# Optimization experiments

Hardware: AMD Instinct MI355X
Metric: run time of the kernel (lower is better)

## Reference

```python
import jax, jax.numpy as jnp
import numpy as np

D = 768          # hidden_size
M = 8            # num_patchmerges
B = 16
S = 2048         # non-CLF tokens


def setup_inputs() -> dict:
    key = jax.random.key(0)
    ks = jax.random.split(key, 12)
    std = 0.02
    tokens = jax.random.normal(ks[0], (B, 1 + S, D), dtype=jnp.float32)
    lengths = jnp.maximum(jax.random.randint(ks[1], (B,), 0, S), 1).astype(jnp.int64)
    # PatchMerger: learned queries + layernorm params
    q = jax.random.normal(ks[2], (M, D), dtype=jnp.float32) * std
    ln_scale = jnp.ones((D,), dtype=jnp.float32)
    ln_bias = jnp.zeros((D,), dtype=jnp.float32)
    # mlp1: Linear(3D, D) -> GELU -> Linear(D, D)
    w1a = jax.random.normal(ks[3], (3 * D, D), dtype=jnp.float32) * std
    b1a = jnp.zeros((D,), dtype=jnp.float32)
    w2a = jax.random.normal(ks[4], (D, D), dtype=jnp.float32) * std
    b2a = jnp.zeros((D,), dtype=jnp.float32)
    # mlp2: Linear((1+M)D, D) -> GELU -> Linear(D, D)
    w1b = jax.random.normal(ks[5], ((1 + M) * D, D), dtype=jnp.float32) * std
    b1b = jnp.zeros((D,), dtype=jnp.float32)
    w2b = jax.random.normal(ks[6], (D, D), dtype=jnp.float32) * std
    b2b = jnp.zeros((D,), dtype=jnp.float32)
    return dict(tokens=tokens, lengths=lengths, q=q, ln_scale=ln_scale,
                ln_bias=ln_bias, w1a=w1a, b1a=b1a, w2a=w2a, b2a=b2a,
                w1b=w1b, b1b=b1b, w2b=w2b, b2b=b2b)


def _hpmlp(x, w1, b1, w2, b2):
    h = jax.nn.gelu(x @ w1 + b1, approximate=False)  # dropout=0 -> identity
    return h @ w2 + b2


def _layernorm(x, scale, bias, eps=1e-5):
    mu = jnp.mean(x, axis=-1, keepdims=True)
    var = jnp.var(x, axis=-1, keepdims=True)
    return (x - mu) * jax.lax.rsqrt(var + eps) * scale + bias


def reference(tokens, lengths, q, ln_scale, ln_bias,
              w1a, b1a, w2a, b2a, w1b, b1b, w2b, b2b):
    clf = tokens[:, 0]            # [B, D]
    x = tokens[:, 1:]             # [B, S, D]
    mask = jnp.arange(S)[None, :] < lengths[:, None]   # [B, S]
    mf = mask[..., None].astype(x.dtype)

    # fixed path: masked mean / max / min over valid tokens
    denom = lengths.astype(x.dtype)[:, None]
    mean_p = jnp.sum(x * mf, axis=1) / denom
    max_p = jnp.max(jnp.where(mask[..., None], x, -jnp.inf), axis=1)
    min_p = jnp.min(jnp.where(mask[..., None], x, jnp.inf), axis=1)
    pooled_trad = jnp.concatenate([mean_p, max_p, min_p], axis=-1)  # [B, 3D]
    out_fixed = _hpmlp(pooled_trad, w1a, b1a, w2a, b2a)

    # learned path: PatchMerger (masked attention from M learned queries)
    xn = _layernorm(x, ln_scale, ln_bias)
    scores = jnp.einsum('md,bsd->bms', q, xn) / jnp.sqrt(jnp.asarray(D, x.dtype))
    scores = jnp.where(mask[:, None, :], scores, -jnp.inf)
    attn = jax.nn.softmax(scores, axis=-1)                # [B, M, S]
    merged = jnp.einsum('bms,bsd->bmd', attn, x)          # [B, M, D]
    pooled_learn = jnp.concatenate([merged.reshape(B, M * D), clf], axis=-1)
    out_learn = _hpmlp(pooled_learn, w1b, b1b, w2b, b2b)

    return jnp.concatenate([out_fixed, out_learn], axis=-1)  # [B, 2D]
```

## Files before the change

### kernel.cpp

```cpp
#include <hip/hip_runtime.h>
#include <math.h>

#define SD 768
#define SB 16
#define SM 8
#define SS 2048
#define TOK_ROW 2049
#define NEG_INF (-__builtin_inff())

#define OFF_PTRADS  0
#define OFF_PLEARN  36864
#define OFF_LTOT    147456
#define OFF_P1A     147584
#define OFF_P1B     368768
#define OFF_HA      1032320
#define OFF_HB      1044608
#define OFF_CNT     1056896

#define NITEM 512

__device__ __forceinline__ int clen(int v) { return v < 1 ? 1 : (v > SS ? SS : v); }

__device__ __forceinline__ unsigned fenc(float f) {
  unsigned u = __float_as_uint(f);
  return (u & 0x80000000u) ? ~u : (u ^ 0x80000000u);
}
__device__ __forceinline__ float fdec(unsigned u) {
  unsigned i = (u & 0x80000000u) ? (u ^ 0x80000000u) : ~u;
  return __uint_as_float(i);
}

__global__ void k_init(float* __restrict__ ws, float* __restrict__ out,
                       const float* __restrict__ b2a, const float* __restrict__ b2b) {
  int i = blockIdx.x * 256 + threadIdx.x;
  int stride = gridDim.x * 256;
  for (int t = i; t < 147584; t += stride) {
    unsigned v = (t >= 24576 && t < 36864) ? 0xFFFFFFFFu : 0u;
    ((unsigned*)ws)[t] = v;
  }
  for (int t = i; t < 24576; t += stride) {
    int b = t / 1536, r = t - b * 1536;
    out[t] = (r < 768) ? b2a[r] : b2b[r - 768];
  }
  if (i == 0) ((int*)ws)[OFF_CNT] = 0;
}

__global__ __launch_bounds__(512, 1) void k_fused(
    const float* __restrict__ tokens, const int* __restrict__ lengths,
    const float* __restrict__ q, const float* __restrict__ lns,
    const float* __restrict__ lnb, float* __restrict__ ptradS,
    float* __restrict__ plearn, float* __restrict__ ltot,
    int* __restrict__ cnt) {
  __shared__ float q_lds[8][SD];
  __shared__ float O_lds[SM][SD];
  __shared__ float pool_lds[8][3][SD];
  __shared__ float l_lds[8][8];
  __shared__ float qmeta[16];
  __shared__ int item_s;
  int tid = threadIdx.x, w = tid >> 6, lane = tid & 63;
  int mm2 = lane & 3;

  {
    float s1 = 0.f, sb = 0.f;
    #pragma unroll
    for (int g = 0; g < 3; ++g) {
      float4 l4  = *(const float4*)(lns + g * 256 + lane * 4);
      float4 lb4 = *(const float4*)(lnb + g * 256 + lane * 4);
      float4 qv  = *(const float4*)(q + w * SD + g * 256 + lane * 4);
      float4 qs = make_float4(qv.x * l4.x, qv.y * l4.y, qv.z * l4.z, qv.w * l4.w);
      *(float4*)&q_lds[w][g * 256 + lane * 4] = qs;
      s1 += qs.x + qs.y + qs.z + qs.w;
      sb += qv.x * lb4.x + qv.y * lb4.y + qv.z * lb4.z + qv.w * lb4.w;
    }
    #pragma unroll
    for (int o = 32; o; o >>= 1) { s1 += __shfl_xor(s1, o, 64); sb += __shfl_xor(sb, o, 64); }
    if (lane == 0) { qmeta[w] = s1; qmeta[8 + w] = sb; }
  }
  __syncthreads();
  float qs1A = qmeta[mm2],     qs1B = qmeta[4 + mm2];
  float qbA  = qmeta[8 + mm2], qbB  = qmeta[12 + mm2];
  const float KS = 0.03608439182435161f;

  for (;;) {
    __syncthreads();
    if (tid == 0) item_s = atomicAdd(cnt, 1);
    __syncthreads();
    int item = item_s;
    if (item >= NITEM) break;
    int b = item >> 5, c = item & 31;
    int len = clen(lengths[b]);
    int c0 = c * 64;
    if (c0 >= len) continue;

    int srow = c0 + w * 8;
    int smax = len - srow; if (smax > 8) smax = 8; if (smax < 0) smax = 0;
    const float* xrow = tokens + ((size_t)b * TOK_ROW + 1 + srow) * SD;

    float psum[12], pmx[12], pmn[12];
    #pragma unroll
    for (int j = 0; j < 12; ++j) { psum[j] = 0.f; pmx[j] = NEG_INF; pmn[j] = -NEG_INF; }
    float O[8][12];
    #pragma unroll
    for (int m = 0; m < 8; ++m)
      #pragma unroll
      for (int j = 0; j < 12; ++j) O[m][j] = 0.f;
    float lA = 0.f, lB = 0.f;

    float4 nx0 = {}, nx1 = {}, nx2 = {};
    if (smax > 0) {
      nx0 = *(const float4*)(xrow + lane * 4);
      nx1 = *(const float4*)(xrow + 256 + lane * 4);
      nx2 = *(const float4*)(xrow + 512 + lane * 4);
    }
    for (int i = 0; i < smax; ++i) {
      float4 x0 = nx0, x1 = nx1, x2 = nx2;
      if (i + 1 < smax) {
        const float* xq = xrow + (size_t)(i + 1) * SD;
        nx0 = *(const float4*)(xq + lane * 4);
        nx1 = *(const float4*)(xq + 256 + lane * 4);
        nx2 = *(const float4*)(xq + 512 + lane * 4);
      }
      float xv[12] = {x0.x, x0.y, x0.z, x0.w, x1.x, x1.y, x1.z, x1.w,
                      x2.x, x2.y, x2.z, x2.w};
      float s1 = 0.f, s2 = 0.f;
      #pragma unroll
      for (int j = 0; j < 12; ++j) {
        float v = xv[j];
        psum[j] += v;
        pmx[j] = fmaxf(pmx[j], v);
        pmn[j] = fminf(pmn[j], v);
        s1 += v;
        s2 += v * v;
      }
      float d[8];
      #pragma unroll
      for (int m = 0; m < 8; ++m) {
        float4 q0 = *(const float4*)&q_lds[m][lane * 4];
        float4 q1 = *(const float4*)&q_lds[m][256 + lane * 4];
        float4 q2 = *(const float4*)&q_lds[m][512 + lane * 4];
        d[m] = q0.x * xv[0] + q0.y * xv[1] + q0.z * xv[2] + q0.w * xv[3]
             + q1.x * xv[4] + q1.y * xv[5] + q1.z * xv[6] + q1.w * xv[7]
             + q2.x * xv[8] + q2.y * xv[9] + q2.z * xv[10] + q2.w * xv[11];
      }
      #pragma unroll
      for (int o = 1; o <= 2; o <<= 1)
        #pragma unroll
        for (int m = 0; m < 8; ++m) d[m] += __shfl_xor(d[m], o, 64);
      float uA = d[0], uB = d[4];
      #pragma unroll
      for (int m = 1; m < 4; ++m) {
        uA = (mm2 == m) ? d[m] : uA;
        uB = (mm2 == m) ? d[4 + m] : uB;
      }
      #pragma unroll
      for (int o = 4; o <= 32; o <<= 1) {
        uA += __shfl_xor(uA, o, 64);
        uB += __shfl_xor(uB, o, 64);
        s1 += __shfl_xor(s1, o, 64);
        s2 += __shfl_xor(s2, o, 64);
      }
      #pragma unroll
      for (int o = 1; o <= 2; o <<= 1) { s1 += __shfl_xor(s1, o, 64); s2 += __shfl_xor(s2, o, 64); }
      float mu = s1 * (1.f / 768.f);
      float var = s2 * (1.f / 768.f) - mu * mu;
      float rstd = rsqrtf(var + 1e-5f);
      float peA = __expf((rstd * uA - rstd * mu * qs1A + qbA) * KS);
      float peB = __expf((rstd * uB - rstd * mu * qs1B + qbB) * KS);
      lA += peA; lB += peB;
      float pm[8];
      #pragma unroll
      for (int m = 0; m < 4; ++m) {
        pm[m]     = __shfl(peA, m, 4);
        pm[4 + m] = __shfl(peB, m, 4);
      }
      #pragma unroll
      for (int m = 0; m < 8; ++m)
        #pragma unroll
        for (int j = 0; j < 12; ++j) O[m][j] += pm[m] * xv[j];
    }

    if (lane < 4) { l_lds[w][lane] = lA; l_lds[w][4 + lane] = lB; }
    #pragma unroll
    for (int g = 0; g < 3; ++g) {
      int dd = g * 256 + lane * 4;
      *(float4*)&pool_lds[w][0][dd] = make_float4(psum[g*4], psum[g*4+1], psum[g*4+2], psum[g*4+3]);
      *(float4*)&pool_lds[w][1][dd] = make_float4(pmx[g*4], pmx[g*4+1], pmx[g*4+2], pmx[g*4+3]);
      *(float4*)&pool_lds[w][2][dd] = make_float4(pmn[g*4], pmn[g*4+1], pmn[g*4+2], pmn[g*4+3]);
    }
    __syncthreads();

    if (tid < 8) {
      float lt = 0.f;
      #pragma unroll
      for (int ww = 0; ww < 8; ++ww) lt += l_lds[ww][tid];
      atomicAdd(&ltot[b * 8 + tid], lt);
    }

    #pragma unroll
    for (int r = 0; r < 8; ++r) {
      if (w == r) {
        #pragma unroll
        for (int m = 0; m < 8; ++m)
          #pragma unroll
          for (int g = 0; g < 3; ++g) {
            int dd = g * 256 + lane * 4;
            float4 mine = make_float4(O[m][g*4], O[m][g*4+1], O[m][g*4+2], O[m][g*4+3]);
            if (r == 0) {
              *(float4*)&O_lds[m][dd] = mine;
            } else {
              float4 cur = *(float4*)&O_lds[m][dd];
              cur.x += mine.x; cur.y += mine.y; cur.z += mine.z; cur.w += mine.w;
              *(float4*)&O_lds[m][dd] = cur;
            }
          }
      }
      __syncthreads();
    }

    {
      const float* of = &O_lds[0][0];
      for (int j = tid; j < 6144; j += 512)
        atomicAdd(&plearn[(size_t)b * 6912 + j], of[j]);
    }
    for (int j = tid; j < 768; j += 512) {
      float s = 0.f, mx = NEG_INF, mn = -NEG_INF;
      #pragma unroll
      for (int ww = 0; ww < 8; ++ww) {
        s += pool_lds[ww][0][j];
        mx = fmaxf(mx, pool_lds[ww][1][j]);
        mn = fminf(mn, pool_lds[ww][2][j]);
      }
      atomicAdd(&ptradS[b * 768 + j], s);
      atomicMax((unsigned*)&ptradS[12288 + b * 768 + j], fenc(mx));
      atomicMin((unsigned*)&ptradS[24576 + b * 768 + j], fenc(mn));
    }
    if (c == 0)
      for (int dd = tid; dd < 768; dd += 512)
        plearn[(size_t)b * 6912 + 6144 + dd] = tokens[(size_t)b * TOK_ROW * SD + dd];
  }
}

__global__ __launch_bounds__(256) void gemm_partial(
    const float* __restrict__ XA, const float* __restrict__ WA, int ktA, float* __restrict__ PA,
    const float* __restrict__ XB, const float* __restrict__ WB, float* __restrict__ PB,
    const int* __restrict__ lengths, const float* __restrict__ ltot,
    int modeA, int modeB, int epi) {
  int nt = blockIdx.x, ky = blockIdx.y;
  const float *X, *W; float* P; int kt, ktN, mode;
  if (ky < ktA) { X = XA; W = WA; P = PA; kt = ky; ktN = ktA; mode = modeA; }
  else { X = XB; W = WB; P = PB; kt = ky - ktA; ktN = gridDim.y - ktA; mode = modeB; }
  int K = ktN * 128;
  int k0 = kt * 128;
  __shared__ __align__(16) float xt[128 * 20];
  __shared__ float red[4][64][17];
  int tid = threadIdx.x;
  int kk = tid & 127, half = tid >> 7;
  #pragma unroll
  for (int u = 0; u < 8; ++u) {
    int b2 = half * 8 + u;
    float f;
    if (mode == 0) {
      int s = kt / 6;
      f = X[s * 12288 + b2 * 768 + (k0 - s * 768) + kk];
      if (s == 0) f = f / (float)clen(lengths[b2]);
      else        f = fdec(__float_as_uint(f));
    } else if (mode == 1) {
      f = X[b2 * 6912 + k0 + kk];
      if (kt < 48) f = f / ltot[b2 * 8 + (k0 / 768)];
    } else {
      f = X[b2 * K + k0 + kk];
    }
    xt[kk * 20 + b2] = f;
  }
  __syncthreads();
  int w = tid >> 6, lane = tid & 63;
  int n = nt * 64 + lane;
  float acc[16];
  #pragma unroll
  for (int b2 = 0; b2 < 16; ++b2) acc[b2] = 0.f;
  const float* Wp = W + (size_t)k0 * SD + n;
  #pragma unroll 8
  for (int kj = 0; kj < 32; ++kj) {
    int k = w + kj * 4;
    float wv = Wp[(size_t)k * SD];
    const float4* xr = reinterpret_cast<const float4*>(xt + k * 20);
    float4 a0 = xr[0], a1 = xr[1], a2 = xr[2], a3 = xr[3];
    acc[0] += wv * a0.x; acc[1] += wv * a0.y; acc[2] += wv * a0.z; acc[3] += wv * a0.w;
    acc[4] += wv * a1.x; acc[5] += wv * a1.y; acc[6] += wv * a1.z; acc[7] += wv * a1.w;
    acc[8] += wv * a2.x; acc[9] += wv * a2.y; acc[10] += wv * a2.z; acc[11] += wv * a2.w;
    acc[12] += wv * a3.x; acc[13] += wv * a3.y; acc[14] += wv * a3.z; acc[15] += wv * a3.w;
  }
  #pragma unroll
  for (int b2 = 0; b2 < 16; ++b2) red[w][lane][b2] = acc[b2];
  __syncthreads();
  for (int i = tid; i < 1024; i += 256) {
    int nn = i & 63, b2 = i >> 6;
    float r = red[0][nn][b2] + red[1][nn][b2] + red[2][nn][b2] + red[3][nn][b2];
    if (epi == 0) P[(size_t)(kt * 16 + b2) * SD + nt * 64 + nn] = r;
    else          atomicAdd(&P[b2 * 1536 + nt * 64 + nn], r);
  }
}

__global__ void gelu_reduce(const float* __restrict__ PA, const float* __restrict__ b1a,
                            float* __restrict__ HA, const float* __restrict__ PB,
                            const float* __restrict__ b1b, float* __restrict__ HB) {
  int y = blockIdx.y;
  int j = blockIdx.x * 256 + threadIdx.x;
  float r;
  if (y == 0) {
    r = b1a[j % SD];
    #pragma unroll
    for (int kt = 0; kt < 18; ++kt) r += PA[kt * 12288 + j];
    HA[j] = r * 0.5f * (1.f + erff(r * 0.70710678118654752f));
  } else {
    r = b1b[j % SD];
    #pragma unroll
    for (int kt = 0; kt < 54; ++kt) r += PB[kt * 12288 + j];
    HB[j] = r * 0.5f * (1.f + erff(r * 0.70710678118654752f));
  }
}

extern "C" void kernel_launch(void* const* d_in, const int* in_sizes, int n_in,
                              void* d_out, int out_size, void* d_ws, size_t ws_size,
                              hipStream_t stream) {
  const float* tokens = (const float*)d_in[0];
  const int* lengths  = (const int*)d_in[1];
  const float* q      = (const float*)d_in[2];
  const float* lns    = (const float*)d_in[3];
  const float* lnb    = (const float*)d_in[4];
  const float* w1a    = (const float*)d_in[5];
  const float* b1a    = (const float*)d_in[6];
  const float* w2a    = (const float*)d_in[7];
  const float* b2a    = (const float*)d_in[8];
  const float* w1b    = (const float*)d_in[9];
  const float* b1b    = (const float*)d_in[10];
  const float* w2b    = (const float*)d_in[11];
  const float* b2b    = (const float*)d_in[12];
  float* ws  = (float*)d_ws;
  float* out = (float*)d_out;

  float* ptradS = ws + OFF_PTRADS;
  float* plearn = ws + OFF_PLEARN;
  float* ltot   = ws + OFF_LTOT;
  float* p1a    = ws + OFF_P1A;
  float* p1b    = ws + OFF_P1B;
  float* ha     = ws + OFF_HA;
  float* hb     = ws + OFF_HB;
  int*   cnt    = (int*)(ws + OFF_CNT);

  k_init<<<dim3(128), 256, 0, stream>>>(ws, out, b2a, b2b);
  k_fused<<<dim3(256), 512, 0, stream>>>(tokens, lengths, q, lns, lnb,
                                         ptradS, plearn, ltot, cnt);
  gemm_partial<<<dim3(12, 72), 256, 0, stream>>>(ptradS, w1a, 18, p1a,
                                                 plearn, w1b, p1b,
                                                 lengths, ltot, 0, 1, 0);
  gelu_reduce<<<dim3(48, 2), 256, 0, stream>>>(p1a, b1a, ha, p1b, b1b, hb);
  gemm_partial<<<dim3(12, 12), 256, 0, stream>>>(ha, w2a, 6, out,
                                                 hb, w2b, out + 768,
                                                 lengths, ltot, 2, 2, 1);
}
```

Measured before the change: 239.1 us.

## Pin fused blocks to one batch and fold GELU reduce into second GEMM

Each fused block now serves a fixed batch (blockIdx mod 16) and pulls chunks from a per-batch atomic counter. It keeps its accumulators across chunks and does the cross-wave reduction and global atomics once at the end instead of once per chunk, which cuts atomic traffic and per-chunk LDS reductions. The separate gelu_reduce kernel is removed: the second GEMM's tile loader sums the split-K partials, adds the bias and applies GELU inline. The trade-off is that batches with short lengths leave their 16 blocks idle while long batches still have only 16 blocks each, so load balance gets worse. The second GEMM also recomputes the partial reductions redundantly across its tiles.

```diff
diff --git a/kernel.cpp b/kernel.cpp
--- a/kernel.cpp
+++ b/kernel.cpp
@@ -13,11 +13,7 @@
 #define OFF_LTOT    147456
 #define OFF_P1A     147584
 #define OFF_P1B     368768
-#define OFF_HA      1032320
-#define OFF_HB      1044608
-#define OFF_CNT     1056896
-
-#define NITEM 512
+#define OFF_CNT     1032320
 
 __device__ __forceinline__ int clen(int v) { return v < 1 ? 1 : (v > SS ? SS : v); }
 
@@ -42,7 +38,7 @@
     int b = t / 1536, r = t - b * 1536;
     out[t] = (r < 768) ? b2a[r] : b2b[r - 768];
   }
-  if (i == 0) ((int*)ws)[OFF_CNT] = 0;
+  if (i < 16) ((int*)(ws + OFF_CNT))[i] = 0;
 }
 
 __global__ __launch_bounds__(512, 1) void k_fused(
@@ -52,13 +48,15 @@
     float* __restrict__ plearn, float* __restrict__ ltot,
     int* __restrict__ cnt) {
   __shared__ float q_lds[8][SD];
-  __shared__ float O_lds[SM][SD];
-  __shared__ float pool_lds[8][3][SD];
+  __shared__ float scr[8][SD];
   __shared__ float l_lds[8][8];
   __shared__ float qmeta[16];
-  __shared__ int item_s;
+  __shared__ int chunk_s;
   int tid = threadIdx.x, w = tid >> 6, lane = tid & 63;
   int mm2 = lane & 3;
+  int b = blockIdx.x & 15;
+  int len = clen(lengths[b]);
+  int nch = (len + 63) >> 6;
 
   {
     float s1 = 0.f, sb = 0.f;
@@ -81,30 +79,30 @@
   float qbA  = qmeta[8 + mm2], qbB  = qmeta[12 + mm2];
   const float KS = 0.03608439182435161f;
 
+  float psum[12], pmx[12], pmn[12];
+  #pragma unroll
+  for (int j = 0; j < 12; ++j) { psum[j] = 0.f; pmx[j] = NEG_INF; pmn[j] = -NEG_INF; }
+  float O[8][12];
+  #pragma unroll
+  for (int m = 0; m < 8; ++m)
+    #pragma unroll
+    for (int j = 0; j < 12; ++j) O[m][j] = 0.f;
+  float lA = 0.f, lB = 0.f;
+  int ndone = 0;
+  bool have_c0 = false;
+
   for (;;) {
     __syncthreads();
-    if (tid == 0) item_s = atomicAdd(cnt, 1);
-    __syncthreads();
-    int item = item_s;
-    if (item >= NITEM) break;
-    int b = item >> 5, c = item & 31;
-    int len = clen(lengths[b]);
-    int c0 = c * 64;
-    if (c0 >= len) continue;
-
-    int srow = c0 + w * 8;
+    if (tid == 0) chunk_s = atomicAdd(&cnt[b], 1);
+    __syncthreads();
+    int c = chunk_s;
+    if (c >= nch) break;
+    ++ndone;
+    if (c == 0) have_c0 = true;
+
+    int srow = c * 64 + w * 8;
     int smax = len - srow; if (smax > 8) smax = 8; if (smax < 0) smax = 0;
     const float* xrow = tokens + ((size_t)b * TOK_ROW + 1 + srow) * SD;
-
-    float psum[12], pmx[12], pmn[12];
-    #pragma unroll
-    for (int j = 0; j < 12; ++j) { psum[j] = 0.f; pmx[j] = NEG_INF; pmn[j] = -NEG_INF; }
-    float O[8][12];
-    #pragma unroll
-    for (int m = 0; m < 8; ++m)
-      #pragma unroll
-      for (int j = 0; j < 12; ++j) O[m][j] = 0.f;
-    float lA = 0.f, lB = 0.f;
 
     float4 nx0 = {}, nx1 = {}, nx2 = {};
     if (smax > 0) {
@@ -178,77 +176,77 @@
         #pragma unroll
         for (int j = 0; j < 12; ++j) O[m][j] += pm[m] * xv[j];
     }
-
-    if (lane < 4) { l_lds[w][lane] = lA; l_lds[w][4 + lane] = lB; }
+  }
+
+  if (ndone == 0) return;
+
+  #pragma unroll
+  for (int m = 0; m < 8; ++m) {
+    __syncthreads();
+    #pragma unroll
+    for (int g = 0; g < 3; ++g)
+      *(float4*)&scr[w][g * 256 + lane * 4] =
+          make_float4(O[m][g*4], O[m][g*4+1], O[m][g*4+2], O[m][g*4+3]);
+    __syncthreads();
+    for (int ch = tid; ch < 768; ch += 512) {
+      float s = scr[0][ch] + scr[1][ch] + scr[2][ch] + scr[3][ch]
+              + scr[4][ch] + scr[5][ch] + scr[6][ch] + scr[7][ch];
+      atomicAdd(&plearn[(size_t)b * 6912 + m * 768 + ch], s);
+    }
+  }
+  #pragma unroll
+  for (int st = 0; st < 3; ++st) {
+    __syncthreads();
     #pragma unroll
     for (int g = 0; g < 3; ++g) {
       int dd = g * 256 + lane * 4;
-      *(float4*)&pool_lds[w][0][dd] = make_float4(psum[g*4], psum[g*4+1], psum[g*4+2], psum[g*4+3]);
-      *(float4*)&pool_lds[w][1][dd] = make_float4(pmx[g*4], pmx[g*4+1], pmx[g*4+2], pmx[g*4+3]);
-      *(float4*)&pool_lds[w][2][dd] = make_float4(pmn[g*4], pmn[g*4+1], pmn[g*4+2], pmn[g*4+3]);
-    }
-    __syncthreads();
-
-    if (tid < 8) {
-      float lt = 0.f;
-      #pragma unroll
-      for (int ww = 0; ww < 8; ++ww) lt += l_lds[ww][tid];
-      atomicAdd(&ltot[b * 8 + tid], lt);
-    }
-
-    #pragma unroll
-    for (int r = 0; r < 8; ++r) {
-      if (w == r) {
-        #pragma unroll
-        for (int m = 0; m < 8; ++m)
-          #pragma unroll
-          for (int g = 0; g < 3; ++g) {
-            int dd = g * 256 + lane * 4;
-            float4 mine = make_float4(O[m][g*4], O[m][g*4+1], O[m][g*4+2], O[m][g*4+3]);
-            if (r == 0) {
-              *(float4*)&O_lds[m][dd] = mine;
-            } else {
-              float4 cur = *(float4*)&O_lds[m][dd];
-              cur.x += mine.x; cur.y += mine.y; cur.z += mine.z; cur.w += mine.w;
-              *(float4*)&O_lds[m][dd] = cur;
-            }
-          }
-      }
-      __syncthreads();
-    }
-
-    {
-      const float* of = &O_lds[0][0];
-      for (int j = tid; j < 6144; j += 512)
-        atomicAdd(&plearn[(size_t)b * 6912 + j], of[j]);
-    }
-    for (int j = tid; j < 768; j += 512) {
-      float s = 0.f, mx = NEG_INF, mn = -NEG_INF;
-      #pragma unroll
-      for (int ww = 0; ww < 8; ++ww) {
-        s += pool_lds[ww][0][j];
-        mx = fmaxf(mx, pool_lds[ww][1][j]);
-        mn = fminf(mn, pool_lds[ww][2][j]);
-      }
-      atomicAdd(&ptradS[b * 768 + j], s);
-      atomicMax((unsigned*)&ptradS[12288 + b * 768 + j], fenc(mx));
-      atomicMin((unsigned*)&ptradS[24576 + b * 768 + j], fenc(mn));
-    }
-    if (c == 0)
-      for (int dd = tid; dd < 768; dd += 512)
-        plearn[(size_t)b * 6912 + 6144 + dd] = tokens[(size_t)b * TOK_ROW * SD + dd];
-  }
+      float4 v;
+      if (st == 0)      v = make_float4(psum[g*4], psum[g*4+1], psum[g*4+2], psum[g*4+3]);
+      else if (st == 1) v = make_float4(pmx[g*4], pmx[g*4+1], pmx[g*4+2], pmx[g*4+3]);
+      else              v = make_float4(pmn[g*4], pmn[g*4+1], pmn[g*4+2], pmn[g*4+3]);
+      *(float4*)&scr[w][dd] = v;
+    }
+    __syncthreads();
+    for (int ch = tid; ch < 768; ch += 512) {
+      if (st == 0) {
+        float s = scr[0][ch] + scr[1][ch] + scr[2][ch] + scr[3][ch]
+                + scr[4][ch] + scr[5][ch] + scr[6][ch] + scr[7][ch];
+        atomicAdd(&ptradS[b * 768 + ch], s);
+      } else if (st == 1) {
+        float s = fmaxf(fmaxf(fmaxf(scr[0][ch], scr[1][ch]), fmaxf(scr[2][ch], scr[3][ch])),
+                        fmaxf(fmaxf(scr[4][ch], scr[5][ch]), fmaxf(scr[6][ch], scr[7][ch])));
+        atomicMax((unsigned*)&ptradS[12288 + b * 768 + ch], fenc(s));
+      } else {
+        float s = fminf(fminf(fminf(scr[0][ch], scr[1][ch]), fminf(scr[2][ch], scr[3][ch])),
+                        fminf(fminf(scr[4][ch], scr[5][ch]), fminf(scr[6][ch], scr[7][ch])));
+        atomicMin((unsigned*)&ptradS[24576 + b * 768 + ch], fenc(s));
+      }
+    }
+  }
+  __syncthreads();
+  if (lane < 4) { l_lds[w][lane] = lA; l_lds[w][4 + lane] = lB; }
+  __syncthreads();
+  if (tid < 8) {
+    float lt = 0.f;
+    #pragma unroll
+    for (int ww = 0; ww < 8; ++ww) lt += l_lds[ww][tid];
+    atomicAdd(&ltot[b * 8 + tid], lt);
+  }
+  if (have_c0)
+    for (int dd = tid; dd < 768; dd += 512)
+      plearn[(size_t)b * 6912 + 6144 + dd] = tokens[(size_t)b * TOK_ROW * SD + dd];
 }
 
 __global__ __launch_bounds__(256) void gemm_partial(
     const float* __restrict__ XA, const float* __restrict__ WA, int ktA, float* __restrict__ PA,
     const float* __restrict__ XB, const float* __restrict__ WB, float* __restrict__ PB,
     const int* __restrict__ lengths, const float* __restrict__ ltot,
+    const float* __restrict__ bA, const float* __restrict__ bB,
     int modeA, int modeB, int epi) {
   int nt = blockIdx.x, ky = blockIdx.y;
-  const float *X, *W; float* P; int kt, ktN, mode;
-  if (ky < ktA) { X = XA; W = WA; P = PA; kt = ky; ktN = ktA; mode = modeA; }
-  else { X = XB; W = WB; P = PB; kt = ky - ktA; ktN = gridDim.y - ktA; mode = modeB; }
+  const float *X, *W, *bias; float* P; int kt, ktN, mode;
+  if (ky < ktA) { X = XA; W = WA; P = PA; kt = ky; ktN = ktA; mode = modeA; bias = bA; }
+  else { X = XB; W = WB; P = PB; kt = ky - ktA; ktN = gridDim.y - ktA; mode = modeB; bias = bB; }
   int K = ktN * 128;
   int k0 = kt * 128;
   __shared__ __align__(16) float xt[128 * 20];
@@ -268,7 +266,17 @@
       f = X[b2 * 6912 + k0 + kk];
       if (kt < 48) f = f / ltot[b2 * 8 + (k0 / 768)];
     } else {
-      f = X[b2 * K + k0 + kk];
+      int k = k0 + kk;
+      const float* Pp = X + b2 * 768 + k;
+      f = bias[k];
+      if (mode == 3) {
+        #pragma unroll
+        for (int t = 0; t < 18; ++t) f += Pp[t * 12288];
+      } else {
+        #pragma unroll 6
+        for (int t = 0; t < 54; ++t) f += Pp[t * 12288];
+      }
+      f = f * 0.5f * (1.f + erff(f * 0.70710678118654752f));
     }
     xt[kk * 20 + b2] = f;
   }
@@ -298,25 +306,6 @@
     float r = red[0][nn][b2] + red[1][nn][b2] + red[2][nn][b2] + red[3][nn][b2];
     if (epi == 0) P[(size_t)(kt * 16 + b2) * SD + nt * 64 + nn] = r;
     else          atomicAdd(&P[b2 * 1536 + nt * 64 + nn], r);
-  }
-}
-
-__global__ void gelu_reduce(const float* __restrict__ PA, const float* __restrict__ b1a,
-                            float* __restrict__ HA, const float* __restrict__ PB,
-                            const float* __restrict__ b1b, float* __restrict__ HB) {
-  int y = blockIdx.y;
-  int j = blockIdx.x * 256 + threadIdx.x;
-  float r;
-  if (y == 0) {
-    r = b1a[j % SD];
-    #pragma unroll
-    for (int kt = 0; kt < 18; ++kt) r += PA[kt * 12288 + j];
-    HA[j] = r * 0.5f * (1.f + erff(r * 0.70710678118654752f));
-  } else {
-    r = b1b[j % SD];
-    #pragma unroll
-    for (int kt = 0; kt < 54; ++kt) r += PB[kt * 12288 + j];
-    HB[j] = r * 0.5f * (1.f + erff(r * 0.70710678118654752f));
   }
 }
 
@@ -344,8 +333,6 @@
   float* ltot   = ws + OFF_LTOT;
   float* p1a    = ws + OFF_P1A;
   float* p1b    = ws + OFF_P1B;
-  float* ha     = ws + OFF_HA;
-  float* hb     = ws + OFF_HB;
   int*   cnt    = (int*)(ws + OFF_CNT);
 
   k_init<<<dim3(128), 256, 0, stream>>>(ws, out, b2a, b2b);
@@ -353,9 +340,8 @@
                                          ptradS, plearn, ltot, cnt);
   gemm_partial<<<dim3(12, 72), 256, 0, stream>>>(ptradS, w1a, 18, p1a,
                                                  plearn, w1b, p1b,
-                                                 lengths, ltot, 0, 1, 0);
-  gelu_reduce<<<dim3(48, 2), 256, 0, stream>>>(p1a, b1a, ha, p1b, b1b, hb);
-  gemm_partial<<<dim3(12, 12), 256, 0, stream>>>(ha, w2a, 6, out,
-                                                 hb, w2b, out + 768,
-                                                 lengths, ltot, 2, 2, 1);
-}
+                                                 lengths, ltot, b1a, b1b, 0, 1, 0);
+  gemm_partial<<<dim3(12, 12), 256, 0, stream>>>(p1a, w2a, 6, out,
+                                                 p1b, w2b, out + 768,
+                                                 lengths, ltot, b1a, b1b, 3, 4, 1);
+}
```

Result: slower. 290.2 us (+21.4%).
